# Optimization experiments

Measured on AMD Instinct MI355X. Metric: run time of the kernel, lower is better.

The kernel has to match this reference:

```python
import jax, jax.numpy as jnp
import numpy as np


def setup_inputs() -> dict:
    key = jax.random.key(0)
    k0, k1, k2, k3, k4 = jax.random.split(key, 5)
    n, c, s, h, w = 4, 128, 31, 32, 22
    x = jax.random.normal(k0, (n, c, s, h, w), dtype=jnp.float32)
    # 1x1 conv to a single channel == per-pixel dot over channels + scalar bias
    scale = 1.0 / np.sqrt(c).astype(np.float32)
    w1 = jax.random.normal(k1, (c,), dtype=jnp.float32) * scale
    b1 = jax.random.normal(k2, (), dtype=jnp.float32) * 0.01
    w2 = jax.random.normal(k3, (c,), dtype=jnp.float32) * scale
    b2 = jax.random.normal(k4, (), dtype=jnp.float32) * 0.01
    return {"x": x, "w1": w1, "b1": b1, "w2": w2, "b2": b2, "top_k": 16}


def reference(x, w1, b1, w2, b2, top_k):
    n, c, s, h, w = x.shape
    hw = h * w
    ns = n * (s - 1)
    # adjacent-frame pairs; 1x1 conv (C->1) as channel contraction
    X0 = jnp.einsum('ncshw,c->nshw', x[:, :, : s - 1], w1) + b1  # (n, s-1, h, w)
    X1 = jnp.einsum('ncshw,c->nshw', x[:, :, 1:], w2) + b2       # (n, s-1, h, w)
    X0 = X0.reshape(ns, hw)
    X1 = X1.reshape(ns, hw)
    # outer-product scores per frame pair, softmax over last dim
    attention = jax.nn.softmax(X0[:, :, None] * X1[:, None, :], axis=2)  # (ns, hw, hw)
    # top-k values along last dim -> (ns, hw, k); torch .view(ns, k, h, w)
    # is a raw row-major reinterpretation, so a plain reshape is faithful.
    vals, _ = jax.lax.top_k(attention, top_k)
    vals = vals.reshape(n, s - 1, top_k, h, w)
    # trans_out: (n, s-1, k, h, w) -> (n, k, s-1, h, w)
    return jnp.transpose(vals, (0, 2, 1, 3, 4))
```

## Files before the change

kernel.cpp:

```cpp
#include <hip/hip_runtime.h>
#include <math.h>

#define NB   4
#define C    128
#define S    31
#define HW   704
#define T    30
#define NS   120
#define K    16

__global__ __launch_bounds__(256) void conv_kernel(
    const float* __restrict__ x,
    const float* __restrict__ w1, const float* __restrict__ b1p,
    const float* __restrict__ w2, const float* __restrict__ b2p,
    float* __restrict__ A, float* __restrict__ B) {
  const int tid  = threadIdx.x;
  const int lane = tid & 63;
  const int cg   = tid >> 6;
  const int g    = blockIdx.x * 64 + lane;
  const int fr   = g / 176;
  const int f4   = g % 176;
  const int sf   = fr % S;
  const int n    = fr / S;

  const float4* xp =
      (const float4*)(x + (((size_t)(n * C + cg * 32) * S + sf) * HW)) + f4;
  float4 a1 = make_float4(0.f, 0.f, 0.f, 0.f);
  float4 a2 = make_float4(0.f, 0.f, 0.f, 0.f);
#pragma unroll
  for (int c = 0; c < 32; ++c) {
    float4 xv = xp[(size_t)c * (S * HW / 4)];
    const float wa = w1[cg * 32 + c];
    const float wb = w2[cg * 32 + c];
    a1.x = fmaf(xv.x, wa, a1.x); a1.y = fmaf(xv.y, wa, a1.y);
    a1.z = fmaf(xv.z, wa, a1.z); a1.w = fmaf(xv.w, wa, a1.w);
    a2.x = fmaf(xv.x, wb, a2.x); a2.y = fmaf(xv.y, wb, a2.y);
    a2.z = fmaf(xv.z, wb, a2.z); a2.w = fmaf(xv.w, wb, a2.w);
  }
  __shared__ float4 s1[4][64];
  __shared__ float4 s2[4][64];
  s1[cg][lane] = a1;
  s2[cg][lane] = a2;
  __syncthreads();
  if (tid < 64) {
    float4 r1 = s1[0][tid], r2 = s2[0][tid];
#pragma unroll
    for (int u = 1; u < 4; ++u) {
      float4 t1 = s1[u][tid], t2 = s2[u][tid];
      r1.x += t1.x; r1.y += t1.y; r1.z += t1.z; r1.w += t1.w;
      r2.x += t2.x; r2.y += t2.y; r2.z += t2.z; r2.w += t2.w;
    }
    const float bb1 = b1p[0], bb2 = b2p[0];
    r1.x += bb1; r1.y += bb1; r1.z += bb1; r1.w += bb1;
    r2.x += bb2; r2.y += bb2; r2.z += bb2; r2.w += bb2;
    if (sf < T)
      ((float4*)(A + (size_t)(n * T + sf) * HW))[f4] = r1;
    if (sf >= 1)
      ((float4*)(B + (size_t)(n * T + sf - 1) * HW))[f4] = r2;
  }
}

__global__ __launch_bounds__(512) void sort_kernel(
    const float* __restrict__ B,
    float* __restrict__ btop, float* __restrict__ bbot) {
  __shared__ float s[1024];
  const int i   = blockIdx.x;
  const int tid = threadIdx.x;
  const float* bi = B + i * HW;
  for (int q = tid; q < 1024; q += 512)
    s[q] = (q < HW) ? bi[q] : INFINITY;
  __syncthreads();
#pragma unroll 1
  for (int k = 2; k <= 1024; k <<= 1) {
#pragma unroll 1
    for (int j = k >> 1; j > 0; j >>= 1) {
#pragma unroll
      for (int idx = tid; idx < 1024; idx += 512) {
        int ixj = idx ^ j;
        if (ixj > idx) {
          float a = s[idx], b = s[ixj];
          if ((a > b) == ((idx & k) == 0)) { s[idx] = b; s[ixj] = a; }
        }
      }
      __syncthreads();
    }
  }
  if (tid < K) {
    bbot[i * K + tid] = s[tid];
    btop[i * K + tid] = s[HW - 1 - tid];
  }
}

__global__ __launch_bounds__(256) void softmax_topk_kernel(
    const float* __restrict__ A, const float* __restrict__ B,
    const float* __restrict__ btop, const float* __restrict__ bbot,
    float* __restrict__ out) {
  const int lane = threadIdx.x & 63;
  const int wid  = blockIdx.x * 4 + (threadIdx.x >> 6);
  const int i    = wid / 176;
  const int rb   = wid % 176;

  const float st0 = btop[i * K];
  const float sb0 = bbot[i * K];
  const float L2E = 1.4426950408889634f;
  float av[4], a2[4], nm[4], part[4];
#pragma unroll
  for (int u = 0; u < 4; ++u) {
    av[u]   = A[i * HW + rb + u * 176];
    a2[u]   = av[u] * L2E;
    nm[u]   = -((av[u] >= 0.f) ? av[u] * st0 : av[u] * sb0) * L2E;
    part[u] = 0.f;
  }

  const float* __restrict__ bi = B + i * HW;
#pragma unroll
  for (int j = 0; j < 11; ++j) {
    const float bv = bi[j * 64 + lane];
#pragma unroll
    for (int u = 0; u < 4; ++u)
      part[u] += __builtin_amdgcn_exp2f(fmaf(a2[u], bv, nm[u]));
  }
#pragma unroll
  for (int off = 1; off < 64; off <<= 1) {
#pragma unroll
    for (int u = 0; u < 4; ++u)
      part[u] += __shfl_xor(part[u], off, 64);
  }

  if (lane < K) {
    const int n  = i / T;
    const int t  = i % T;
    float* obase = out + (((size_t)n * K) * T + t) * HW;
    const float tv = btop[i * K + lane];
    const float bv = bbot[i * K + lane];
#pragma unroll
    for (int u = 0; u < 4; ++u) {
      const int r = rb + u * 176;
      const float sel = (av[u] >= 0.f) ? tv : bv;
      const float val = __builtin_amdgcn_exp2f(fmaf(a2[u], sel, nm[u])) / part[u];
      obase[(size_t)(r / 44) * (T * HW) + (r % 44) * K + lane] = val;
    }
  }
}

extern "C" void kernel_launch(void* const* d_in, const int* in_sizes, int n_in,
                              void* d_out, int out_size, void* d_ws, size_t ws_size,
                              hipStream_t stream) {
  (void)in_sizes; (void)n_in; (void)out_size; (void)ws_size;
  const float* x  = (const float*)d_in[0];
  const float* w1 = (const float*)d_in[1];
  const float* b1 = (const float*)d_in[2];
  const float* w2 = (const float*)d_in[3];
  const float* b2 = (const float*)d_in[4];
  float* out = (float*)d_out;

  float* A    = (float*)d_ws;
  float* B    = A + NS * HW;
  float* btop = B + NS * HW;
  float* bbot = btop + NS * K;

  conv_kernel<<<341, 256, 0, stream>>>(x, w1, b1, w2, b2, A, B);
  sort_kernel<<<NS, 512, 0, stream>>>(B, btop, bbot);
  softmax_topk_kernel<<<5280, 256, 0, stream>>>(A, B, btop, bbot, out);
}
```

Measured before the change: 119.4 us.

## Replace full bitonic sort with register-based iterative top-k selection per wavefront

The per-frame full bitonic sort of 1024 elements in shared memory, with many block-wide barriers, is replaced by a single-wavefront kernel. Each lane holds 11 values in registers, and it runs 16 rounds of max/min reductions via shuffles and ballots, removing one element per round. This removes the shared-memory traffic and the barriers of the sort stage. In exchange, only 120 single-wave blocks run, so occupancy is low, and the shuffle reductions are serial.

```diff
diff --git a/kernel.cpp b/kernel.cpp
--- a/kernel.cpp
+++ b/kernel.cpp
@@ -60,34 +60,59 @@
   }
 }
 
-__global__ __launch_bounds__(512) void sort_kernel(
+__global__ __launch_bounds__(64) void select_kernel(
     const float* __restrict__ B,
     float* __restrict__ btop, float* __restrict__ bbot) {
-  __shared__ float s[1024];
-  const int i   = blockIdx.x;
-  const int tid = threadIdx.x;
-  const float* bi = B + i * HW;
-  for (int q = tid; q < 1024; q += 512)
-    s[q] = (q < HW) ? bi[q] : INFINITY;
-  __syncthreads();
+  const int i    = blockIdx.x;
+  const int lane = threadIdx.x;
+  const float* __restrict__ bi = B + i * HW;
+
+  float vt[11], vb[11];
+#pragma unroll
+  for (int j = 0; j < 11; ++j) {
+    const float v = bi[j * 64 + lane];
+    vt[j] = v;
+    vb[j] = v;
+  }
+
 #pragma unroll 1
-  for (int k = 2; k <= 1024; k <<= 1) {
-#pragma unroll 1
-    for (int j = k >> 1; j > 0; j >>= 1) {
+  for (int r = 0; r < K; ++r) {
+    float lmT = vt[0], lmB = vb[0];
 #pragma unroll
-      for (int idx = tid; idx < 1024; idx += 512) {
-        int ixj = idx ^ j;
-        if (ixj > idx) {
-          float a = s[idx], b = s[ixj];
-          if ((a > b) == ((idx & k) == 0)) { s[idx] = b; s[ixj] = a; }
-        }
+    for (int j = 1; j < 11; ++j) {
+      lmT = fmaxf(lmT, vt[j]);
+      lmB = fminf(lmB, vb[j]);
+    }
+    float gT = lmT, gB = lmB;
+#pragma unroll
+    for (int off = 1; off < 64; off <<= 1) {
+      gT = fmaxf(gT, __shfl_xor(gT, off, 64));
+      gB = fminf(gB, __shfl_xor(gB, off, 64));
+    }
+    const unsigned long long mT = __ballot(lmT == gT);
+    const unsigned long long mB = __ballot(lmB == gB);
+    if (lane == (int)(__ffsll(mT) - 1)) {
+      bool done = false;
+#pragma unroll
+      for (int j = 0; j < 11; ++j) {
+        const bool hit = (!done) && (vt[j] == gT);
+        vt[j] = hit ? -INFINITY : vt[j];
+        done  = done || hit;
       }
-      __syncthreads();
     }
-  }
-  if (tid < K) {
-    bbot[i * K + tid] = s[tid];
-    btop[i * K + tid] = s[HW - 1 - tid];
+    if (lane == (int)(__ffsll(mB) - 1)) {
+      bool done = false;
+#pragma unroll
+      for (int j = 0; j < 11; ++j) {
+        const bool hit = (!done) && (vb[j] == gB);
+        vb[j] = hit ? INFINITY : vb[j];
+        done  = done || hit;
+      }
+    }
+    if (lane == 0) {
+      btop[i * K + r] = gT;
+      bbot[i * K + r] = gB;
+    }
   }
 }
 
@@ -160,6 +185,6 @@
   float* bbot = btop + NS * K;
 
   conv_kernel<<<341, 256, 0, stream>>>(x, w1, b1, w2, b2, A, B);
-  sort_kernel<<<NS, 512, 0, stream>>>(B, btop, bbot);
+  select_kernel<<<NS, 64, 0, stream>>>(B, btop, bbot);
   softmax_topk_kernel<<<5280, 256, 0, stream>>>(A, B, btop, bbot, out);
 }
```

Measured after the change: 115.3 us. 1.04x faster.
